# Performance work log

Measured on AMD Instinct MI355X. Metric: run time of the kernel, lower is better.

The kernel has to match this reference:

```python
import jax, jax.numpy as jnp
import numpy as np

COMPRESSION = 2  # max-pool factor along flattened spatial axis for phi and g


def setup_inputs() -> dict:
    key = jax.random.key(0)
    ks = jax.random.split(key, 5)
    B, C, H, W = 4, 64, 96, 96
    Ci = 32  # intermediate_dim = C // 2
    s = 1.0 / np.sqrt(C)
    return {
        "x": jax.random.normal(ks[0], (B, C, H, W), dtype=jnp.float32),
        "w_theta": jax.random.normal(ks[1], (Ci, C), dtype=jnp.float32) * s,
        "b_theta": jnp.zeros((Ci,), dtype=jnp.float32),
        "w_phi": jax.random.normal(ks[2], (Ci, C), dtype=jnp.float32) * s,
        "b_phi": jnp.zeros((Ci,), dtype=jnp.float32),
        "w_g": jax.random.normal(ks[3], (Ci, C), dtype=jnp.float32) * s,
        "b_g": jnp.zeros((Ci,), dtype=jnp.float32),
        "w_out": jax.random.normal(ks[4], (C, Ci), dtype=jnp.float32) * (1.0 / np.sqrt(Ci)),
        "b_out": jnp.zeros((C,), dtype=jnp.float32),
    }


def reference(x, w_theta, b_theta, w_phi, b_phi, w_g, b_g, w_out, b_out):
    B, C, H, W = x.shape
    N = H * W
    xf = x.reshape(B, C, N).transpose(0, 2, 1)            # [B, N, C]
    # 1x1 conv projections == channel matmuls
    theta = xf @ w_theta.T + b_theta                      # [B, N, Ci]
    phi = xf @ w_phi.T + b_phi                            # [B, N, Ci]
    g = xf @ w_g.T + b_g                                  # [B, N, Ci]
    # compression: max-pool (kernel=stride=COMPRESSION) along flattened spatial axis
    Ci = theta.shape[-1]
    phi = phi.reshape(B, N // COMPRESSION, COMPRESSION, Ci).max(axis=2)  # [B, N/c, Ci]
    g = g.reshape(B, N // COMPRESSION, COMPRESSION, Ci).max(axis=2)      # [B, N/c, Ci]
    # embedded-gaussian affinity + softmax
    attn = jax.nn.softmax(jnp.einsum('bnc,bmc->bnm', theta, phi), axis=-1)  # [B, N, N/c]
    y = jnp.einsum('bnm,bmc->bnc', attn, g)               # [B, N, Ci]
    out = y @ w_out.T + b_out                             # [B, N, C]
    out = out.transpose(0, 2, 1).reshape(B, C, H, W)
    return out + x  # residual
```

## Files before the change

kernel.cpp:

```cpp
#include <hip/hip_runtime.h>
#include <hip/hip_bf16.h>


#define NQ 9216
#define MM 4608
#define LOG2E 1.44269504088896340736f

typedef __attribute__((ext_vector_type(8))) short bf16x8;
typedef __attribute__((ext_vector_type(4))) float f32x4;
typedef __attribute__((ext_vector_type(4))) unsigned short u16x4;

static __device__ __forceinline__ unsigned pk2(float a, float b) {
    __hip_bfloat162 h = __float22bfloat162_rn(make_float2(a, b));
    return *reinterpret_cast<unsigned*>(&h);
}

__global__ __launch_bounds__(128, 4) void proj_kernel(
    const float* __restrict__ x,
    const float* __restrict__ wt, const float* __restrict__ bt,
    const float* __restrict__ wp, const float* __restrict__ bp,
    const float* __restrict__ wg, const float* __restrict__ bg,
    unsigned short* __restrict__ theta, unsigned short* __restrict__ phi,
    unsigned short* __restrict__ gT, float* __restrict__ pzero)
{
    __shared__ unsigned short gst[32 * 20];

    const int tid  = threadIdx.x;
    const int wid  = tid >> 6;
    const int lane = tid & 63;
    const int q = lane >> 4;
    const int c = lane & 15;

    {
        const int gs = gridDim.x * blockDim.x;
        float4 z4 = {0.f, 0.f, 0.f, 0.f};
        for (int i = blockIdx.x * blockDim.x + tid; i < 304128; i += gs)
            ((float4*)pzero)[i] = z4;
    }

    const int b     = blockIdx.x / 288;
    const int rem   = blockIdx.x % 288;
    const int n0blk = rem * 32;
    const int n0    = n0blk + wid * 16;

    const float* Wm[3] = {wt, wp, wg};
    const float* Bm[3] = {bt, bp, bg};

    bf16x8 wf[3][2][2];
    float bias[3][2];
#pragma unroll
    for (int p = 0; p < 3; ++p) {
#pragma unroll
        for (int ct = 0; ct < 2; ++ct) {
            bias[p][ct] = Bm[p][ct * 16 + c];
#pragma unroll
            for (int ks = 0; ks < 2; ++ks) {
                const float* wsrc = Wm[p] + (ct * 16 + c) * 64 + ks * 32 + q * 8;
                f32x4 w0 = *(const f32x4*)wsrc;
                f32x4 w1 = *(const f32x4*)(wsrc + 4);
                unsigned* wk = (unsigned*)&wf[p][ct][ks];
                wk[0] = pk2(w0[0], w0[1]); wk[1] = pk2(w0[2], w0[3]);
                wk[2] = pk2(w1[0], w1[1]); wk[3] = pk2(w1[2], w1[3]);
            }
        }
    }

    bf16x8 af[2];
#pragma unroll
    for (int ks = 0; ks < 2; ++ks) {
        unsigned* ap = (unsigned*)&af[ks];
#pragma unroll
        for (int j2 = 0; j2 < 4; ++j2) {
            float x0 = x[(b * 64 + ks * 32 + q * 8 + j2 * 2) * NQ + n0 + c];
            float x1 = x[(b * 64 + ks * 32 + q * 8 + j2 * 2 + 1) * NQ + n0 + c];
            ap[j2] = pk2(x0, x1);
        }
    }

#pragma unroll
    for (int p = 0; p < 3; ++p) {
#pragma unroll
        for (int ct = 0; ct < 2; ++ct) {
            f32x4 acc = {0.f, 0.f, 0.f, 0.f};
            acc = __builtin_amdgcn_mfma_f32_16x16x32_bf16(af[0], wf[p][ct][0], acc, 0, 0, 0);
            acc = __builtin_amdgcn_mfma_f32_16x16x32_bf16(af[1], wf[p][ct][1], acc, 0, 0, 0);
#pragma unroll
            for (int r = 0; r < 4; ++r) acc[r] += bias[p][ct];
            const int ci = ct * 16 + c;
            if (p == 0) {
                unsigned pv0 = pk2(acc[0] * LOG2E, acc[1] * LOG2E);
                unsigned pv1 = pk2(acc[2] * LOG2E, acc[3] * LOG2E);
                theta[(b * NQ + n0 + 4 * q + 0) * 32 + ci] = (unsigned short)pv0;
                theta[(b * NQ + n0 + 4 * q + 1) * 32 + ci] = (unsigned short)(pv0 >> 16);
                theta[(b * NQ + n0 + 4 * q + 2) * 32 + ci] = (unsigned short)pv1;
                theta[(b * NQ + n0 + 4 * q + 3) * 32 + ci] = (unsigned short)(pv1 >> 16);
            } else {
                unsigned pv = pk2(fmaxf(acc[0], acc[1]), fmaxf(acc[2], acc[3]));
                if (p == 1) {
                    const int m0 = (n0 >> 1) + 2 * q;
                    phi[(b * MM + m0) * 32 + ci]     = (unsigned short)pv;
                    phi[(b * MM + m0 + 1) * 32 + ci] = (unsigned short)(pv >> 16);
                } else {
                    *(unsigned int*)(gst + ci * 20 + wid * 8 + 2 * q) = pv;
                }
            }
        }
    }

    __syncthreads();
    {
        const int ci = tid >> 2;
        const int m4 = (tid & 3) * 4;
        u16x4 v = *(const u16x4*)(gst + ci * 20 + m4);
        *(u16x4*)(gT + (b * 32 + ci) * MM + rem * 16 + m4) = v;
    }
}

__global__ __launch_bounds__(128, 3) void attn_kernel(
    const unsigned short* __restrict__ theta, const unsigned short* __restrict__ phi,
    const unsigned short* __restrict__ gT,
    float* __restrict__ pacc, float* __restrict__ plsum)
{
    __shared__ unsigned short pld[2][64 * 64];

    const int tid  = threadIdx.x;
    const int w    = tid >> 6;
    const int lane = tid & 63;
    const int q  = lane >> 4;
    const int c  = lane & 15;
    const int xr = (c & 7) << 3;

    const int ks  = blockIdx.x / 288;
    const int rem = blockIdx.x % 288;
    const int b   = rem / 72;
    const int nb  = (rem % 72) * 128 + w * 64;

    bf16x8 qf[4];
#pragma unroll
    for (int rt = 0; rt < 4; ++rt)
        qf[rt] = *(const bf16x8*)(theta + (b * NQ + nb + rt * 16 + c) * 32 + q * 8);

    bf16x8 onef;
    {
        unsigned v = (c == 0) ? 0x3F803F80u : 0u;
        unsigned* op = (unsigned*)&onef;
        op[0] = v; op[1] = v; op[2] = v; op[3] = v;
    }

    const unsigned short* phiB = phi + (size_t)b * MM * 32;
    const unsigned short* gTB  = gT + (size_t)b * 32 * MM;
    unsigned short* myp = pld[w];

    f32x4 acc[4][2];
    f32x4 lacc[4];
#pragma unroll
    for (int rt = 0; rt < 4; ++rt) {
        lacc[rt] = (f32x4){0.f, 0.f, 0.f, 0.f};
#pragma unroll
        for (int s2 = 0; s2 < 2; ++s2) acc[rt][s2] = (f32x4){0.f, 0.f, 0.f, 0.f};
    }

    const int mt0 = ks * 9;
    bf16x8 kf[4], vf[2][2];

#pragma unroll
    for (int mct = 0; mct < 4; ++mct)
        kf[mct] = *(const bf16x8*)(phiB + (mt0 * 64 + mct * 16 + c) * 32 + q * 8);
#pragma unroll
    for (int s2 = 0; s2 < 2; ++s2)
#pragma unroll
        for (int st = 0; st < 2; ++st)
            vf[s2][st] = *(const bf16x8*)(gTB + (s2 * 16 + c) * MM + mt0 * 64 + st * 32 + q * 8);
#pragma unroll
    for (int mct = 0; mct < 4; ++mct) {
#pragma unroll
        for (int rt = 0; rt < 4; ++rt) {
            f32x4 z = {0.f, 0.f, 0.f, 0.f};
            f32x4 s = __builtin_amdgcn_mfma_f32_16x16x32_bf16(kf[mct], qf[rt], z, 0, 0, 0);
            uint2 hv = {pk2(__builtin_amdgcn_exp2f(s[0]), __builtin_amdgcn_exp2f(s[1])),
                        pk2(__builtin_amdgcn_exp2f(s[2]), __builtin_amdgcn_exp2f(s[3]))};
            *(uint2*)(myp + ((rt * 16 + c) << 6) + ((mct * 16 + 4 * q) ^ xr)) = hv;
        }
    }

    for (int mi = 1; mi < 9; ++mi) {
        const int m0 = (mt0 + mi) * 64;

#pragma unroll
        for (int mct = 0; mct < 4; ++mct)
            kf[mct] = *(const bf16x8*)(phiB + (m0 + mct * 16 + c) * 32 + q * 8);

#pragma unroll
        for (int rt = 0; rt < 4; ++rt) {
#pragma unroll
            for (int st = 0; st < 2; ++st) {
                bf16x8 pf = *(const bf16x8*)(myp + ((rt * 16 + c) << 6) + ((st * 32 + q * 8) ^ xr));
#pragma unroll
                for (int s2 = 0; s2 < 2; ++s2)
                    acc[rt][s2] = __builtin_amdgcn_mfma_f32_16x16x32_bf16(vf[s2][st], pf, acc[rt][s2], 0, 0, 0);
                lacc[rt] = __builtin_amdgcn_mfma_f32_16x16x32_bf16(onef, pf, lacc[rt], 0, 0, 0);
            }
        }

#pragma unroll
        for (int s2 = 0; s2 < 2; ++s2)
#pragma unroll
            for (int st = 0; st < 2; ++st)
                vf[s2][st] = *(const bf16x8*)(gTB + (s2 * 16 + c) * MM + m0 + st * 32 + q * 8);

#pragma unroll
        for (int mct = 0; mct < 4; ++mct) {
#pragma unroll
            for (int rt = 0; rt < 4; ++rt) {
                f32x4 z = {0.f, 0.f, 0.f, 0.f};
                f32x4 s = __builtin_amdgcn_mfma_f32_16x16x32_bf16(kf[mct], qf[rt], z, 0, 0, 0);
                uint2 hv = {pk2(__builtin_amdgcn_exp2f(s[0]), __builtin_amdgcn_exp2f(s[1])),
                            pk2(__builtin_amdgcn_exp2f(s[2]), __builtin_amdgcn_exp2f(s[3]))};
                *(uint2*)(myp + ((rt * 16 + c) << 6) + ((mct * 16 + 4 * q) ^ xr)) = hv;
            }
        }
    }

#pragma unroll
    for (int rt = 0; rt < 4; ++rt) {
#pragma unroll
        for (int st = 0; st < 2; ++st) {
            bf16x8 pf = *(const bf16x8*)(myp + ((rt * 16 + c) << 6) + ((st * 32 + q * 8) ^ xr));
#pragma unroll
            for (int s2 = 0; s2 < 2; ++s2)
                acc[rt][s2] = __builtin_amdgcn_mfma_f32_16x16x32_bf16(vf[s2][st], pf, acc[rt][s2], 0, 0, 0);
            lacc[rt] = __builtin_amdgcn_mfma_f32_16x16x32_bf16(onef, pf, lacc[rt], 0, 0, 0);
        }
    }

#pragma unroll
    for (int rt = 0; rt < 4; ++rt)
#pragma unroll
        for (int s2 = 0; s2 < 2; ++s2)
#pragma unroll
            for (int r = 0; r < 4; ++r)
                atomicAdd(&pacc[(size_t)(b * 32 + s2 * 16 + 4 * q + r) * NQ + nb + rt * 16 + c],
                          acc[rt][s2][r]);
    if (lane < 16) {
#pragma unroll
        for (int rt = 0; rt < 4; ++rt)
            atomicAdd(&plsum[(size_t)b * NQ + nb + rt * 16 + lane], lacc[rt][0]);
    }
}

__global__ __launch_bounds__(128, 4) void reduce_kernel(
    const float* __restrict__ pacc, const float* __restrict__ plsum,
    const float* __restrict__ w_out, const float* __restrict__ b_out,
    const float* __restrict__ x, float* __restrict__ out)
{
    __shared__ unsigned short yld[32 * 36];

    const int tid = threadIdx.x;
    const int b   = blockIdx.x / 288;
    const int nb  = (blockIdx.x % 288) * 32;

    {
        const int ci = tid >> 2;
        const int n8 = (tid & 3) * 8;
        const float* pr = pacc + (size_t)(b * 32 + ci) * NQ + nb + n8;
        f32x4 a0 = *(const f32x4*)pr;
        f32x4 a1 = *(const f32x4*)(pr + 4);
        const float* lr = plsum + (size_t)b * NQ + nb + n8;
        f32x4 l0 = *(const f32x4*)lr;
        f32x4 l1 = *(const f32x4*)(lr + 4);
        uint2 v0 = {pk2(a0[0] / l0[0], a0[1] / l0[1]), pk2(a0[2] / l0[2], a0[3] / l0[3])};
        uint2 v1 = {pk2(a1[0] / l1[0], a1[1] / l1[1]), pk2(a1[2] / l1[2], a1[3] / l1[3])};
        *(uint2*)(yld + ci * 36 + n8)     = v0;
        *(uint2*)(yld + ci * 36 + n8 + 4) = v1;
    }
    __syncthreads();

    const int w    = tid >> 6;
    const int lane = tid & 63;
    const int q = lane >> 4;
    const int c = lane & 15;

    bf16x8 wof[4];
#pragma unroll
    for (int ct = 0; ct < 4; ++ct) {
        const float* wsrc = w_out + (ct * 16 + c) * 32 + q * 8;
        f32x4 w0 = *(const f32x4*)wsrc;
        f32x4 w1 = *(const f32x4*)(wsrc + 4);
        unsigned* wk = (unsigned*)&wof[ct];
        wk[0] = pk2(w0[0], w0[1]); wk[1] = pk2(w0[2], w0[3]);
        wk[2] = pk2(w1[0], w1[1]); wk[3] = pk2(w1[2], w1[3]);
    }

    bf16x8 yf;
    {
        unsigned short* yp = (unsigned short*)&yf;
#pragma unroll
        for (int j = 0; j < 8; ++j)
            yp[j] = yld[(q * 8 + j) * 36 + w * 16 + c];
    }

#pragma unroll
    for (int ct = 0; ct < 4; ++ct) {
        f32x4 z = {0.f, 0.f, 0.f, 0.f};
        f32x4 o = __builtin_amdgcn_mfma_f32_16x16x32_bf16(wof[ct], yf, z, 0, 0, 0);
#pragma unroll
        for (int r = 0; r < 4; ++r) {
            const int chn = ct * 16 + 4 * q + r;
            const size_t addr = (size_t)(b * 64 + chn) * NQ + nb + w * 16 + c;
            out[addr] = o[r] + b_out[chn] + x[addr];
        }
    }
}

extern "C" void kernel_launch(void* const* d_in, const int* in_sizes, int n_in,
                              void* d_out, int out_size, void* d_ws, size_t ws_size,
                              hipStream_t stream) {
    const float* x       = (const float*)d_in[0];
    const float* w_theta = (const float*)d_in[1];
    const float* b_theta = (const float*)d_in[2];
    const float* w_phi   = (const float*)d_in[3];
    const float* b_phi   = (const float*)d_in[4];
    const float* w_g     = (const float*)d_in[5];
    const float* b_g     = (const float*)d_in[6];
    const float* w_out   = (const float*)d_in[7];
    const float* b_out   = (const float*)d_in[8];
    float* out = (float*)d_out;

    unsigned short* theta = (unsigned short*)d_ws;
    unsigned short* phi   = theta + 4 * NQ * 32;
    unsigned short* gT    = phi + 4 * MM * 32;
    float* pacc  = (float*)(gT + 4 * 32 * MM);
    float* plsum = pacc + (size_t)4 * 32 * NQ;

    proj_kernel<<<1152, 128, 0, stream>>>(x, w_theta, b_theta, w_phi, b_phi,
                                          w_g, b_g, theta, phi, gT, pacc);
    attn_kernel<<<8 * 288, 128, 0, stream>>>(theta, phi, gT, pacc, plsum);
    reduce_kernel<<<1152, 128, 0, stream>>>(pacc, plsum, w_out, b_out, x, out);
}
```

Measured before the change: 142.7 us.

## Split projection waves by role and raise attention split-K count

The projection kernel moves to 256-thread blocks. Two waves compute theta while two waves compute phi and g, so each wave holds fewer weight fragments in registers and more waves run in parallel. The attention kernel splits the key range into 12 chunks of 6 tiles instead of 8 chunks of 9, launches more blocks, and raises its launch-bounds occupancy hint from 3 to 4. This adds parallelism and latency hiding, at the cost of more partial-sum accumulation traffic into pacc/plsum and possible register pressure under the tighter occupancy bound.

```diff
diff --git a/kernel.cpp b/kernel.cpp
--- a/kernel.cpp
+++ b/kernel.cpp
@@ -15,7 +15,7 @@
     return *reinterpret_cast<unsigned*>(&h);
 }
 
-__global__ __launch_bounds__(128, 4) void proj_kernel(
+__global__ __launch_bounds__(256, 4) void proj_kernel(
     const float* __restrict__ x,
     const float* __restrict__ wt, const float* __restrict__ bt,
     const float* __restrict__ wp, const float* __restrict__ bp,
@@ -30,6 +30,8 @@
     const int lane = tid & 63;
     const int q = lane >> 4;
     const int c = lane & 15;
+    const int role = wid >> 1;
+    const int sub  = wid & 1;
 
     {
         const int gs = gridDim.x * blockDim.x;
@@ -41,29 +43,7 @@
     const int b     = blockIdx.x / 288;
     const int rem   = blockIdx.x % 288;
     const int n0blk = rem * 32;
-    const int n0    = n0blk + wid * 16;
-
-    const float* Wm[3] = {wt, wp, wg};
-    const float* Bm[3] = {bt, bp, bg};
-
-    bf16x8 wf[3][2][2];
-    float bias[3][2];
-#pragma unroll
-    for (int p = 0; p < 3; ++p) {
-#pragma unroll
-        for (int ct = 0; ct < 2; ++ct) {
-            bias[p][ct] = Bm[p][ct * 16 + c];
-#pragma unroll
-            for (int ks = 0; ks < 2; ++ks) {
-                const float* wsrc = Wm[p] + (ct * 16 + c) * 64 + ks * 32 + q * 8;
-                f32x4 w0 = *(const f32x4*)wsrc;
-                f32x4 w1 = *(const f32x4*)(wsrc + 4);
-                unsigned* wk = (unsigned*)&wf[p][ct][ks];
-                wk[0] = pk2(w0[0], w0[1]); wk[1] = pk2(w0[2], w0[3]);
-                wk[2] = pk2(w1[0], w1[1]); wk[3] = pk2(w1[2], w1[3]);
-            }
-        }
-    }
+    const int n0    = n0blk + sub * 16;
 
     bf16x8 af[2];
 #pragma unroll
@@ -77,46 +57,88 @@
         }
     }
 
-#pragma unroll
-    for (int p = 0; p < 3; ++p) {
+    if (role == 0) {
+        bf16x8 wf[2][2];
+        float bias[2];
+#pragma unroll
+        for (int ct = 0; ct < 2; ++ct) {
+            bias[ct] = bt[ct * 16 + c];
+#pragma unroll
+            for (int ks = 0; ks < 2; ++ks) {
+                const float* wsrc = wt + (ct * 16 + c) * 64 + ks * 32 + q * 8;
+                f32x4 w0 = *(const f32x4*)wsrc;
+                f32x4 w1 = *(const f32x4*)(wsrc + 4);
+                unsigned* wk = (unsigned*)&wf[ct][ks];
+                wk[0] = pk2(w0[0], w0[1]); wk[1] = pk2(w0[2], w0[3]);
+                wk[2] = pk2(w1[0], w1[1]); wk[3] = pk2(w1[2], w1[3]);
+            }
+        }
 #pragma unroll
         for (int ct = 0; ct < 2; ++ct) {
             f32x4 acc = {0.f, 0.f, 0.f, 0.f};
-            acc = __builtin_amdgcn_mfma_f32_16x16x32_bf16(af[0], wf[p][ct][0], acc, 0, 0, 0);
-            acc = __builtin_amdgcn_mfma_f32_16x16x32_bf16(af[1], wf[p][ct][1], acc, 0, 0, 0);
-#pragma unroll
-            for (int r = 0; r < 4; ++r) acc[r] += bias[p][ct];
+            acc = __builtin_amdgcn_mfma_f32_16x16x32_bf16(af[0], wf[ct][0], acc, 0, 0, 0);
+            acc = __builtin_amdgcn_mfma_f32_16x16x32_bf16(af[1], wf[ct][1], acc, 0, 0, 0);
             const int ci = ct * 16 + c;
-            if (p == 0) {
-                unsigned pv0 = pk2(acc[0] * LOG2E, acc[1] * LOG2E);
-                unsigned pv1 = pk2(acc[2] * LOG2E, acc[3] * LOG2E);
-                theta[(b * NQ + n0 + 4 * q + 0) * 32 + ci] = (unsigned short)pv0;
-                theta[(b * NQ + n0 + 4 * q + 1) * 32 + ci] = (unsigned short)(pv0 >> 16);
-                theta[(b * NQ + n0 + 4 * q + 2) * 32 + ci] = (unsigned short)pv1;
-                theta[(b * NQ + n0 + 4 * q + 3) * 32 + ci] = (unsigned short)(pv1 >> 16);
-            } else {
+            unsigned pv0 = pk2((acc[0] + bias[ct]) * LOG2E, (acc[1] + bias[ct]) * LOG2E);
+            unsigned pv1 = pk2((acc[2] + bias[ct]) * LOG2E, (acc[3] + bias[ct]) * LOG2E);
+            theta[(b * NQ + n0 + 4 * q + 0) * 32 + ci] = (unsigned short)pv0;
+            theta[(b * NQ + n0 + 4 * q + 1) * 32 + ci] = (unsigned short)(pv0 >> 16);
+            theta[(b * NQ + n0 + 4 * q + 2) * 32 + ci] = (unsigned short)pv1;
+            theta[(b * NQ + n0 + 4 * q + 3) * 32 + ci] = (unsigned short)(pv1 >> 16);
+        }
+    } else {
+        const float* Wm[2] = {wp, wg};
+        const float* Bm[2] = {bp, bg};
+        bf16x8 wf[2][2][2];
+        float bias[2][2];
+#pragma unroll
+        for (int p = 0; p < 2; ++p) {
+#pragma unroll
+            for (int ct = 0; ct < 2; ++ct) {
+                bias[p][ct] = Bm[p][ct * 16 + c];
+#pragma unroll
+                for (int ks = 0; ks < 2; ++ks) {
+                    const float* wsrc = Wm[p] + (ct * 16 + c) * 64 + ks * 32 + q * 8;
+                    f32x4 w0 = *(const f32x4*)wsrc;
+                    f32x4 w1 = *(const f32x4*)(wsrc + 4);
+                    unsigned* wk = (unsigned*)&wf[p][ct][ks];
+                    wk[0] = pk2(w0[0], w0[1]); wk[1] = pk2(w0[2], w0[3]);
+                    wk[2] = pk2(w1[0], w1[1]); wk[3] = pk2(w1[2], w1[3]);
+                }
+            }
+        }
+#pragma unroll
+        for (int p = 0; p < 2; ++p) {
+#pragma unroll
+            for (int ct = 0; ct < 2; ++ct) {
+                f32x4 acc = {0.f, 0.f, 0.f, 0.f};
+                acc = __builtin_amdgcn_mfma_f32_16x16x32_bf16(af[0], wf[p][ct][0], acc, 0, 0, 0);
+                acc = __builtin_amdgcn_mfma_f32_16x16x32_bf16(af[1], wf[p][ct][1], acc, 0, 0, 0);
+#pragma unroll
+                for (int r = 0; r < 4; ++r) acc[r] += bias[p][ct];
+                const int ci = ct * 16 + c;
                 unsigned pv = pk2(fmaxf(acc[0], acc[1]), fmaxf(acc[2], acc[3]));
-                if (p == 1) {
+                if (p == 0) {
                     const int m0 = (n0 >> 1) + 2 * q;
                     phi[(b * MM + m0) * 32 + ci]     = (unsigned short)pv;
                     phi[(b * MM + m0 + 1) * 32 + ci] = (unsigned short)(pv >> 16);
                 } else {
-                    *(unsigned int*)(gst + ci * 20 + wid * 8 + 2 * q) = pv;
+                    *(unsigned int*)(gst + ci * 20 + sub * 8 + 2 * q) = pv;
                 }
             }
         }
     }
 
     __syncthreads();
-    {
+    if (tid < 128) {
         const int ci = tid >> 2;
         const int m4 = (tid & 3) * 4;
         u16x4 v = *(const u16x4*)(gst + ci * 20 + m4);
-        *(u16x4*)(gT + (b * 32 + ci) * MM + rem * 16 + m4) = v;
-    }
-}
-
-__global__ __launch_bounds__(128, 3) void attn_kernel(
+        *(u16x4*)(gT + (b * 32 + ci) * MM + (n0blk >> 1) + m4) = v;
+    }
+}
+
+__global__ __launch_bounds__(128, 4) void attn_kernel(
     const unsigned short* __restrict__ theta, const unsigned short* __restrict__ phi,
     const unsigned short* __restrict__ gT,
     float* __restrict__ pacc, float* __restrict__ plsum)
@@ -160,7 +182,7 @@
         for (int s2 = 0; s2 < 2; ++s2) acc[rt][s2] = (f32x4){0.f, 0.f, 0.f, 0.f};
     }
 
-    const int mt0 = ks * 9;
+    const int mt0 = ks * 6;
     bf16x8 kf[4], vf[2][2];
 
 #pragma unroll
@@ -183,7 +205,7 @@
         }
     }
 
-    for (int mi = 1; mi < 9; ++mi) {
+    for (int mi = 1; mi < 6; ++mi) {
         const int m0 = (mt0 + mi) * 64;
 
 #pragma unroll
@@ -332,8 +354,8 @@
     float* pacc  = (float*)(gT + 4 * 32 * MM);
     float* plsum = pacc + (size_t)4 * 32 * NQ;
 
-    proj_kernel<<<1152, 128, 0, stream>>>(x, w_theta, b_theta, w_phi, b_phi,
+    proj_kernel<<<1152, 256, 0, stream>>>(x, w_theta, b_theta, w_phi, b_phi,
                                           w_g, b_g, theta, phi, gT, pacc);
-    attn_kernel<<<8 * 288, 128, 0, stream>>>(theta, phi, gT, pacc, plsum);
+    attn_kernel<<<12 * 288, 128, 0, stream>>>(theta, phi, gT, pacc, plsum);
     reduce_kernel<<<1152, 128, 0, stream>>>(pacc, plsum, w_out, b_out, x, out);
 }
```

Measured after the change: 151.4 us. 1.06x slower.
